# Kernel optimization log

Hardware: AMD Instinct MI355X
Metric: run time of the kernel (lower is better)

The kernel has to match this reference:

```python
import jax, jax.numpy as jnp
import numpy as np

B, C, CI, H, W = 8, 256, 64, 64, 64  # batch, in_channels, inter_channels, spatial


def conv1x1(x, w, b):
    # x: [B,C,H,W], w: [O,C] (1x1 kernel), b: [O]
    return jnp.einsum('bchw,oc->bohw', x, w) + b[None, :, None, None]


def setup_inputs() -> dict:
    key = jax.random.key(0)
    ks = jax.random.split(key, 9)
    s_in = 1.0 / np.sqrt(C)
    s_ci = 1.0 / np.sqrt(CI)
    return {
        'x': jax.random.normal(ks[0], (B, C, H, W), dtype=jnp.float32),
        'g_w': jax.random.uniform(ks[1], (CI, C), jnp.float32, -s_in, s_in),
        'g_b': jax.random.uniform(ks[2], (CI,), jnp.float32, -s_in, s_in),
        'theta_w': jax.random.uniform(ks[3], (CI, C), jnp.float32, -s_in, s_in),
        'theta_b': jax.random.uniform(ks[4], (CI,), jnp.float32, -s_in, s_in),
        'phi_w': jax.random.uniform(ks[5], (CI, C), jnp.float32, -s_in, s_in),
        'phi_b': jax.random.uniform(ks[6], (CI,), jnp.float32, -s_in, s_in),
        'w_w': jax.random.uniform(ks[7], (C, CI), jnp.float32, -s_ci, s_ci),
        'w_b': jax.random.uniform(ks[8], (C,), jnp.float32, -s_ci, s_ci),
    }


def reference(x, g_w, g_b, theta_w, theta_b, phi_w, phi_b, w_w, w_b):
    b, c, h, w = x.shape
    n = h * w
    # 1x1 conv projections, flattened over spatial positions -> [B, N, CI]
    g_x = conv1x1(x, g_w, g_b).reshape(b, CI, n).transpose(0, 2, 1)
    theta_x = conv1x1(x, theta_w, theta_b).reshape(b, CI, n).transpose(0, 2, 1)
    phi_x = conv1x1(x, phi_w, phi_b).reshape(b, CI, n)  # [B, CI, N]
    # Full non-scaled attention over spatial positions
    f = jnp.einsum('bnc,bcm->bnm', theta_x, phi_x)       # [B, N, N]
    f_div_c = jax.nn.softmax(f, axis=-1)
    y = jnp.einsum('bnm,bmc->bnc', f_div_c, g_x)         # [B, N, CI]
    y = y.transpose(0, 2, 1).reshape(b, CI, h, w)
    w_y = conv1x1(y, w_w, w_b)                            # [B, C, H, W]
    return w_y + x
```

## Files before the change

kernel.cpp:

```cpp
#include <hip/hip_runtime.h>
#include <hip/hip_bf16.h>

#define B_  8
#define C_  256
#define CI_ 64
#define N_  4096
#define KSPLIT 4
#define KTILES (N_ / 64 / KSPLIT)

typedef short short8  __attribute__((ext_vector_type(8)));
typedef short sh4     __attribute__((ext_vector_type(4)));
typedef float floatx4 __attribute__((ext_vector_type(4)));

#define LOG2E 1.4426950408889634f

__device__ __forceinline__ unsigned short f2bf(float f) {
    unsigned u = __builtin_bit_cast(unsigned, f);
    u += 0x7FFFu + ((u >> 16) & 1u);
    return (unsigned short)(u >> 16);
}
__device__ __forceinline__ float bf2f(unsigned short h) {
    unsigned u = ((unsigned)h) << 16;
    return __builtin_bit_cast(float, u);
}

__device__ __forceinline__ unsigned pk2(float a, float b) {
#if __has_builtin(__builtin_amdgcn_cvt_pk_bf16_f32)
    auto r = __builtin_amdgcn_cvt_pk_bf16_f32(a, b);
    return __builtin_bit_cast(unsigned, r);
#else
    return (unsigned)f2bf(a) | ((unsigned)f2bf(b) << 16);
#endif
}

__device__ __forceinline__ floatx4 mfma32(short8 a, short8 b, floatx4 c) {
    return __builtin_amdgcn_mfma_f32_16x16x32_bf16(a, b, c, 0, 0, 0);
}
__device__ __forceinline__ floatx4 mfma16(sh4 a, sh4 b, floatx4 c) {
#if __has_builtin(__builtin_amdgcn_mfma_f32_16x16x16bf16_1k)
    return __builtin_amdgcn_mfma_f32_16x16x16bf16_1k(a, b, c, 0, 0, 0);
#else
    floatx4 d;
    asm("v_mfma_f32_16x16x16_bf16 %0, %1, %2, %3" : "=v"(d) : "v"(a), "v"(b), "v"(c));
    return d;
#endif
}

__global__ __launch_bounds__(512, 4) void proj_kernel(
    const float* __restrict__ x,
    const float* __restrict__ wg, const float* __restrict__ bg,
    const float* __restrict__ wt, const float* __restrict__ bt,
    const float* __restrict__ wp, const float* __restrict__ bp,
    unsigned short* __restrict__ gws,
    unsigned short* __restrict__ tws,
    unsigned short* __restrict__ pws)
{
    constexpr int WS = 40;
    constexpr int GS = 72;
    __shared__ __align__(16) unsigned short wsl[2][192 * WS];
    __shared__ __align__(16) unsigned short gt[64 * GS];

    const int t    = threadIdx.x;
    const int lane = t & 63;
    const int w    = t >> 6;
    const int nf   = w >> 1;
    const int oh   = w & 1;
    const int l15  = lane & 15;
    const int quad = lane >> 4;
    const int n0   = blockIdx.x * 64;
    const int b    = blockIdx.y;

    floatx4 acc[6];
#pragma unroll
    for (int i = 0; i < 6; ++i) { floatx4 z = {0.f, 0.f, 0.f, 0.f}; acc[i] = z; }

    const int nA = n0 + nf * 16 + l15;
    const float* xbase = x + (size_t)b * C_ * N_ + nA;

    float xv[64];
#pragma unroll
    for (int kk = 0; kk < 8; ++kk)
#pragma unroll
        for (int j = 0; j < 8; ++j)
            xv[kk * 8 + j] = xbase[(size_t)(kk * 32 + quad * 8 + j) * N_];

#pragma unroll
    for (int it = 0; it < 3; ++it) {
        int u = t + it * 512;
        int row = u >> 3, c4 = u & 7;
        const float* src = (row < 64)  ? (wg + row * C_)
                         : (row < 128) ? (wt + (row - 64) * C_)
                                       : (wp + (row - 128) * C_);
        const float sc = (row >= 64 && row < 128) ? LOG2E : 1.0f;
        float4 v = *(const float4*)(src + c4 * 4);
        uint2 uu = { pk2(v.x * sc, v.y * sc), pk2(v.z * sc, v.w * sc) };
        *(uint2*)&wsl[0][row * WS + c4 * 4] = uu;
    }
    __syncthreads();

    for (int kk = 0; kk < 8; ++kk) {
        uint4 au = { pk2(xv[kk * 8 + 0], xv[kk * 8 + 1]),
                     pk2(xv[kk * 8 + 2], xv[kk * 8 + 3]),
                     pk2(xv[kk * 8 + 4], xv[kk * 8 + 5]),
                     pk2(xv[kk * 8 + 6], xv[kk * 8 + 7]) };
        short8 af = __builtin_bit_cast(short8, au);

        if (kk < 7) {
#pragma unroll
            for (int it = 0; it < 3; ++it) {
                int u = t + it * 512;
                int row = u >> 3, c4 = u & 7;
                const float* src = (row < 64)  ? (wg + row * C_)
                                 : (row < 128) ? (wt + (row - 64) * C_)
                                               : (wp + (row - 128) * C_);
                const float sc = (row >= 64 && row < 128) ? LOG2E : 1.0f;
                float4 v = *(const float4*)(src + (kk + 1) * 32 + c4 * 4);
                uint2 uu = { pk2(v.x * sc, v.y * sc), pk2(v.z * sc, v.w * sc) };
                *(uint2*)&wsl[(kk + 1) & 1][row * WS + c4 * 4] = uu;
            }
        }

#pragma unroll
        for (int oti = 0; oti < 6; ++oti) {
            const int ot = oh * 6 + oti;
            short8 bf = *(const short8*)&wsl[kk & 1][(ot * 16 + l15) * WS + quad * 8];
            acc[oti] = mfma32(af, bf, acc[oti]);
        }
        __syncthreads();
    }

#pragma unroll
    for (int oti = 0; oti < 6; ++oti) {
        const int ot = oh * 6 + oti;
        const int oc = ot * 16 + l15;
        const float bias = (ot < 4) ? bg[oc]
                         : (ot < 8) ? bt[oc - 64] * LOG2E
                                    : bp[oc - 128];
        if (ot < 4) {
#pragma unroll
            for (int r = 0; r < 4; ++r)
                gt[oc * GS + nf * 16 + quad * 4 + r] = f2bf(acc[oti][r] + bias);
        } else {
            unsigned short* dst = (ot < 8) ? tws : pws;
            const int ci = (ot < 8) ? (oc - 64) : (oc - 128);
#pragma unroll
            for (int r = 0; r < 4; ++r) {
                int n = n0 + nf * 16 + quad * 4 + r;
                dst[((size_t)b * N_ + n) * CI_ + ci] = f2bf(acc[oti][r] + bias);
            }
        }
    }
    __syncthreads();
    {
        int ci = t >> 3, n8 = t & 7;
        uint4 v = *(const uint4*)&gt[ci * GS + n8 * 8];
        *(uint4*)(gws + ((size_t)b * CI_ + ci) * N_ + n0 + n8 * 8) = v;
    }
}

__global__ __launch_bounds__(256, 4) void attn_kernel(
    const unsigned short* __restrict__ gws,
    const unsigned short* __restrict__ tws,
    const unsigned short* __restrict__ pws,
    unsigned short* __restrict__ Opart,
    float* __restrict__ lpart)
{
    constexpr int LDW = 72;
    __shared__ __align__(16) unsigned short Vs[2][64 * LDW];

    const int t    = threadIdx.x;
    const int lane = t & 63;
    const int w    = t >> 6;
    const int l15  = lane & 15;
    const int quad = lane >> 4;
    const int b    = blockIdx.x;
    const int q0   = blockIdx.y * 128;
    const int sp   = blockIdx.z;

    const int srow = t >> 3;
    const int sc8  = t & 7;

    const unsigned short* kslice = pws + ((size_t)b * N_ + sp * (N_ / KSPLIT)) * CI_;
    const unsigned short* vbase  =
        gws + ((size_t)b * CI_ + srow) * N_ + sp * (N_ / KSPLIT) + sc8 * 8;

    short8 qf[2][2];
#pragma unroll
    for (int qg = 0; qg < 2; ++qg) {
        const unsigned short* qrow =
            tws + ((size_t)b * N_ + q0 + w * 32 + qg * 16 + l15) * CI_;
        qf[qg][0] = *(const short8*)(qrow + quad * 8);
        qf[qg][1] = *(const short8*)(qrow + 32 + quad * 8);
    }

    {
        uint4 v0 = *(const uint4*)(vbase);
        uint4 v1 = *(const uint4*)(vbase + 32 * N_);
        *(uint4*)&Vs[0][srow * LDW + sc8 * 8]        = v0;
        *(uint4*)&Vs[0][(srow + 32) * LDW + sc8 * 8] = v1;
    }
    __syncthreads();

    sh4 ones4;
#pragma unroll
    for (int j = 0; j < 4; ++j) ones4[j] = (short)0x3F80;

    floatx4 Oacc[2][4], lacc[2];
    { floatx4 z = {0.f, 0.f, 0.f, 0.f};
      lacc[0] = z; lacc[1] = z;
#pragma unroll
      for (int qg = 0; qg < 2; ++qg)
#pragma unroll
          for (int f = 0; f < 4; ++f) Oacc[qg][f] = z; }

    for (int j = 0; j < KTILES; ++j) {
        const int p  = j & 1;
        const int jn = (j + 1) & (KTILES - 1);

        uint4 pv0 = *(const uint4*)(vbase + jn * 64);
        uint4 pv1 = *(const uint4*)(vbase + 32 * N_ + jn * 64);

        const unsigned short* kt = kslice + (size_t)j * 64 * CI_;
        short8 ka[4][2];
#pragma unroll
        for (int f = 0; f < 4; ++f) {
            ka[f][0] = *(const short8*)(kt + (f * 16 + l15) * CI_ + quad * 8);
            ka[f][1] = *(const short8*)(kt + (f * 16 + l15) * CI_ + 32 + quad * 8);
        }

#pragma unroll
        for (int f = 0; f < 4; ++f) {
            sh4 pfr[2];
#pragma unroll
            for (int qg = 0; qg < 2; ++qg) {
                floatx4 s = {0.f, 0.f, 0.f, 0.f};
                s = mfma32(ka[f][0], qf[qg][0], s);
                s = mfma32(ka[f][1], qf[qg][1], s);
                uint2 uu = { pk2(__builtin_amdgcn_exp2f(s[0]),
                                 __builtin_amdgcn_exp2f(s[1])),
                             pk2(__builtin_amdgcn_exp2f(s[2]),
                                 __builtin_amdgcn_exp2f(s[3])) };
                pfr[qg] = __builtin_bit_cast(sh4, uu);
                lacc[qg] = mfma16(pfr[qg], ones4, lacc[qg]);
            }
#pragma unroll
            for (int fc = 0; fc < 4; ++fc) {
                sh4 vb = *(const sh4*)&Vs[p][(fc * 16 + l15) * LDW + f * 16 + quad * 4];
#pragma unroll
                for (int qg = 0; qg < 2; ++qg)
                    Oacc[qg][fc] = mfma16(pfr[qg], vb, Oacc[qg][fc]);
            }
        }

        *(uint4*)&Vs[1 - p][srow * LDW + sc8 * 8]        = pv0;
        *(uint4*)&Vs[1 - p][(srow + 32) * LDW + sc8 * 8] = pv1;

        __syncthreads();
    }

#pragma unroll
    for (int qg = 0; qg < 2; ++qg) {
#pragma unroll
        for (int r = 0; r < 4; ++r) {
            int row = q0 + w * 32 + qg * 16 + quad * 4 + r;
            size_t obase = ((size_t)(sp * B_ + b) * N_ + row) * CI_;
#pragma unroll
            for (int fc = 0; fc < 4; ++fc)
                Opart[obase + fc * 16 + l15] = f2bf(Oacc[qg][fc][r]);
            if (l15 == 0)
                lpart[(size_t)(sp * B_ + b) * N_ + row] = lacc[qg][r];
        }
    }
}

__global__ __launch_bounds__(256, 4) void out_kernel(
    const unsigned short* __restrict__ Opart,
    const float* __restrict__ lpart,
    const float* __restrict__ ww,
    const float* __restrict__ wb,
    const float* __restrict__ x,
    float* __restrict__ out)
{
    constexpr int WS = 72;
    constexpr int TS = 66;
    __shared__ __align__(16) char smem[128 * TS * 4];
    unsigned short* wws = (unsigned short*)smem;
    float*          T   = (float*)smem;

    const int t    = threadIdx.x;
    const int lane = t & 63;
    const int w    = t >> 6;
    const int l15  = lane & 15;
    const int quad = lane >> 4;
    const int n0   = blockIdx.x * 64;
    const int b    = blockIdx.y;
    const int ch   = blockIdx.z;

#pragma unroll
    for (int it = 0; it < 8; ++it) {
        int u = t + it * 256;
        int row = u >> 4, c4 = u & 15;
        float4 v = *(const float4*)(ww + (ch * 128 + row) * CI_ + c4 * 4);
        uint2 uu = { pk2(v.x, v.y), pk2(v.z, v.w) };
        *(uint2*)&wws[row * WS + c4 * 4] = uu;
    }
    __syncthreads();

    floatx4 acc[8];
#pragma unroll
    for (int ot = 0; ot < 8; ++ot) { floatx4 z = {0.f, 0.f, 0.f, 0.f}; acc[ot] = z; }

    const int nB = n0 + w * 16 + l15;
    float lsum = 0.f;
#pragma unroll
    for (int sp = 0; sp < KSPLIT; ++sp)
        lsum += lpart[(size_t)(sp * B_ + b) * N_ + nB];
    const float inv = 1.f / lsum;

#pragma unroll
    for (int ks = 0; ks < 2; ++ks) {
        float ysum[8] = {0.f, 0.f, 0.f, 0.f, 0.f, 0.f, 0.f, 0.f};
#pragma unroll
        for (int sp = 0; sp < KSPLIT; ++sp) {
            short8 ov = *(const short8*)(Opart +
                ((size_t)(sp * B_ + b) * N_ + nB) * CI_ + ks * 32 + quad * 8);
#pragma unroll
            for (int e = 0; e < 8; ++e)
                ysum[e] += bf2f((unsigned short)ov[e]);
        }
        uint4 bu = { pk2(ysum[0] * inv, ysum[1] * inv),
                     pk2(ysum[2] * inv, ysum[3] * inv),
                     pk2(ysum[4] * inv, ysum[5] * inv),
                     pk2(ysum[6] * inv, ysum[7] * inv) };
        short8 bfrag = __builtin_bit_cast(short8, bu);
#pragma unroll
        for (int ot = 0; ot < 8; ++ot) {
            short8 afrag = *(const short8*)&wws[(ot * 16 + l15) * WS + ks * 32 + quad * 8];
            acc[ot] = mfma32(afrag, bfrag, acc[ot]);
        }
    }
    __syncthreads();

#pragma unroll
    for (int ot = 0; ot < 8; ++ot) {
#pragma unroll
        for (int r = 0; r < 4; ++r) {
            int cr = ot * 16 + quad * 4 + r;
            T[cr * TS + w * 16 + l15] = acc[ot][r] + wb[ch * 128 + cr];
        }
    }
    __syncthreads();

    const int c0 = t >> 4;
    const int nq = t & 15;
#pragma unroll
    for (int i = 0; i < 8; ++i) {
        int cr = c0 + 16 * i;
        float4 tv = *(const float4*)&T[cr * TS + nq * 4];
        size_t idx = ((size_t)b * C_ + ch * 128 + cr) * N_ + n0 + nq * 4;
        float4 xv = *(const float4*)(x + idx);
        float4 ov = { tv.x + xv.x, tv.y + xv.y, tv.z + xv.z, tv.w + xv.w };
        *(float4*)(out + idx) = ov;
    }
}

extern "C" void kernel_launch(void* const* d_in, const int* in_sizes, int n_in,
                              void* d_out, int out_size, void* d_ws, size_t ws_size,
                              hipStream_t stream) {
    const float* x  = (const float*)d_in[0];
    const float* gw = (const float*)d_in[1];
    const float* gb = (const float*)d_in[2];
    const float* tw = (const float*)d_in[3];
    const float* tb = (const float*)d_in[4];
    const float* pw = (const float*)d_in[5];
    const float* pb = (const float*)d_in[6];
    const float* ww = (const float*)d_in[7];
    const float* wb = (const float*)d_in[8];
    float* out = (float*)d_out;

    char* ws = (char*)d_ws;
    unsigned short* gws   = (unsigned short*)(ws);
    unsigned short* tws   = (unsigned short*)(ws + (4  << 20));
    unsigned short* pws   = (unsigned short*)(ws + (8  << 20));
    unsigned short* Opart = (unsigned short*)(ws + (12 << 20));
    float*          lpart = (float*)        (ws + (28 << 20));

    proj_kernel<<<dim3(64, 8), 512, 0, stream>>>(x, gw, gb, tw, tb, pw, pb, gws, tws, pws);
    attn_kernel<<<dim3(8, 32, KSPLIT), 256, 0, stream>>>(gws, tws, pws, Opart, lpart);
    out_kernel<<<dim3(64, 8, 2), 256, 0, stream>>>(Opart, lpart, ww, wb, x, out);
}
```

Baseline: 187.7 us.

## Restructure projection and output kernels to smaller tiles; prefetch K in attention

The projection kernel now works on 32-position tiles with 256 threads. It stages a transposed bf16 copy of x in shared memory and streams weight rows from global memory straight into registers, replacing the previous register-held x with shared-memory weights. The attention kernel software-pipelines the K fragment loads: the next tile's K is fetched after the current scores are exponentiated, to hide global-load latency. The output kernel also moves to 32-position tiles with a 2x2 warp split, doubling the grid for more parallelism. The cost is more blocks, reloading weights per block, and higher register pressure from the buffered fragments.

Result: slower. 209.2 us (+11.5%).

```diff
diff --git a/kernel.cpp b/kernel.cpp
--- a/kernel.cpp
+++ b/kernel.cpp
@@ -23,7 +23,6 @@
     unsigned u = ((unsigned)h) << 16;
     return __builtin_bit_cast(float, u);
 }
-
 __device__ __forceinline__ unsigned pk2(float a, float b) {
 #if __has_builtin(__builtin_amdgcn_cvt_pk_bf16_f32)
     auto r = __builtin_amdgcn_cvt_pk_bf16_f32(a, b);
@@ -32,7 +31,11 @@
     return (unsigned)f2bf(a) | ((unsigned)f2bf(b) << 16);
 #endif
 }
-
+__device__ __forceinline__ short8 pack8(float4 a, float4 b, float sc) {
+    uint4 u = { pk2(a.x * sc, a.y * sc), pk2(a.z * sc, a.w * sc),
+                pk2(b.x * sc, b.y * sc), pk2(b.z * sc, b.w * sc) };
+    return __builtin_bit_cast(short8, u);
+}
 __device__ __forceinline__ floatx4 mfma32(short8 a, short8 b, floatx4 c) {
     return __builtin_amdgcn_mfma_f32_16x16x32_bf16(a, b, c, 0, 0, 0);
 }
@@ -46,7 +49,7 @@
 #endif
 }
 
-__global__ __launch_bounds__(512, 4) void proj_kernel(
+__global__ __launch_bounds__(256, 4) void proj_kernel(
     const float* __restrict__ x,
     const float* __restrict__ wg, const float* __restrict__ bg,
     const float* __restrict__ wt, const float* __restrict__ bt,
@@ -55,106 +58,119 @@
     unsigned short* __restrict__ tws,
     unsigned short* __restrict__ pws)
 {
-    constexpr int WS = 40;
-    constexpr int GS = 72;
-    __shared__ __align__(16) unsigned short wsl[2][192 * WS];
+    constexpr int XK = 40;
+    constexpr int GS = 40;
+    __shared__ __align__(16) unsigned short xt[2][32 * XK];
     __shared__ __align__(16) unsigned short gt[64 * GS];
 
     const int t    = threadIdx.x;
     const int lane = t & 63;
     const int w    = t >> 6;
-    const int nf   = w >> 1;
-    const int oh   = w & 1;
     const int l15  = lane & 15;
     const int quad = lane >> 4;
-    const int n0   = blockIdx.x * 64;
+    const int n0   = blockIdx.x * 32;
     const int b    = blockIdx.y;
 
-    floatx4 acc[6];
-#pragma unroll
-    for (int i = 0; i < 6; ++i) { floatx4 z = {0.f, 0.f, 0.f, 0.f}; acc[i] = z; }
-
-    const int nA = n0 + nf * 16 + l15;
-    const float* xbase = x + (size_t)b * C_ * N_ + nA;
-
-    float xv[64];
-#pragma unroll
-    for (int kk = 0; kk < 8; ++kk)
-#pragma unroll
-        for (int j = 0; j < 8; ++j)
-            xv[kk * 8 + j] = xbase[(size_t)(kk * 32 + quad * 8 + j) * N_];
-
-#pragma unroll
-    for (int it = 0; it < 3; ++it) {
-        int u = t + it * 512;
-        int row = u >> 3, c4 = u & 7;
-        const float* src = (row < 64)  ? (wg + row * C_)
-                         : (row < 128) ? (wt + (row - 64) * C_)
-                                       : (wp + (row - 128) * C_);
-        const float sc = (row >= 64 && row < 128) ? LOG2E : 1.0f;
-        float4 v = *(const float4*)(src + c4 * 4);
-        uint2 uu = { pk2(v.x * sc, v.y * sc), pk2(v.z * sc, v.w * sc) };
-        *(uint2*)&wsl[0][row * WS + c4 * 4] = uu;
-    }
+    const float* wrow[3];
+    float wsc[3];
+    int   frag[3];
+#pragma unroll
+    for (int of = 0; of < 3; ++of) {
+        int fr = w * 3 + of;
+        frag[of] = fr;
+        if (fr < 4)      { wrow[of] = wg + (fr * 16 + l15) * C_;          wsc[of] = 1.0f; }
+        else if (fr < 8) { wrow[of] = wt + ((fr - 4) * 16 + l15) * C_;    wsc[of] = LOG2E; }
+        else             { wrow[of] = wp + ((fr - 8) * 16 + l15) * C_;    wsc[of] = 1.0f; }
+    }
+
+    floatx4 acc[3][2];
+#pragma unroll
+    for (int of = 0; of < 3; ++of)
+#pragma unroll
+        for (int nf = 0; nf < 2; ++nf) { floatx4 z = {0.f,0.f,0.f,0.f}; acc[of][nf] = z; }
+
+    const int xr = t >> 3;
+    const int xc = t & 7;
+    const float* xsrc = x + ((size_t)b * C_ + xr) * N_ + n0 + xc * 4;
+
+    float4 xv = *(const float4*)(xsrc);
+    float4 wcur[3][2];
+#pragma unroll
+    for (int of = 0; of < 3; ++of) {
+        wcur[of][0] = *(const float4*)(wrow[of] + quad * 8);
+        wcur[of][1] = *(const float4*)(wrow[of] + quad * 8 + 4);
+    }
+    xt[0][(xc * 4 + 0) * XK + xr] = f2bf(xv.x);
+    xt[0][(xc * 4 + 1) * XK + xr] = f2bf(xv.y);
+    xt[0][(xc * 4 + 2) * XK + xr] = f2bf(xv.z);
+    xt[0][(xc * 4 + 3) * XK + xr] = f2bf(xv.w);
     __syncthreads();
 
     for (int kk = 0; kk < 8; ++kk) {
-        uint4 au = { pk2(xv[kk * 8 + 0], xv[kk * 8 + 1]),
-                     pk2(xv[kk * 8 + 2], xv[kk * 8 + 3]),
-                     pk2(xv[kk * 8 + 4], xv[kk * 8 + 5]),
-                     pk2(xv[kk * 8 + 6], xv[kk * 8 + 7]) };
-        short8 af = __builtin_bit_cast(short8, au);
-
+        float4 xn;
+        float4 wn[3][2];
         if (kk < 7) {
-#pragma unroll
-            for (int it = 0; it < 3; ++it) {
-                int u = t + it * 512;
-                int row = u >> 3, c4 = u & 7;
-                const float* src = (row < 64)  ? (wg + row * C_)
-                                 : (row < 128) ? (wt + (row - 64) * C_)
-                                               : (wp + (row - 128) * C_);
-                const float sc = (row >= 64 && row < 128) ? LOG2E : 1.0f;
-                float4 v = *(const float4*)(src + (kk + 1) * 32 + c4 * 4);
-                uint2 uu = { pk2(v.x * sc, v.y * sc), pk2(v.z * sc, v.w * sc) };
-                *(uint2*)&wsl[(kk + 1) & 1][row * WS + c4 * 4] = uu;
+            xn = *(const float4*)(xsrc + (size_t)(kk + 1) * 32 * N_);
+#pragma unroll
+            for (int of = 0; of < 3; ++of) {
+                wn[of][0] = *(const float4*)(wrow[of] + (kk + 1) * 32 + quad * 8);
+                wn[of][1] = *(const float4*)(wrow[of] + (kk + 1) * 32 + quad * 8 + 4);
             }
         }
 
-#pragma unroll
-        for (int oti = 0; oti < 6; ++oti) {
-            const int ot = oh * 6 + oti;
-            short8 bf = *(const short8*)&wsl[kk & 1][(ot * 16 + l15) * WS + quad * 8];
-            acc[oti] = mfma32(af, bf, acc[oti]);
+        short8 bf[3];
+#pragma unroll
+        for (int of = 0; of < 3; ++of)
+            bf[of] = pack8(wcur[of][0], wcur[of][1], wsc[of]);
+
+#pragma unroll
+        for (int nf = 0; nf < 2; ++nf) {
+            short8 af = *(const short8*)&xt[kk & 1][(nf * 16 + l15) * XK + quad * 8];
+#pragma unroll
+            for (int of = 0; of < 3; ++of)
+                acc[of][nf] = mfma32(af, bf[of], acc[of][nf]);
+        }
+
+        if (kk < 7) {
+            xt[(kk + 1) & 1][(xc * 4 + 0) * XK + xr] = f2bf(xn.x);
+            xt[(kk + 1) & 1][(xc * 4 + 1) * XK + xr] = f2bf(xn.y);
+            xt[(kk + 1) & 1][(xc * 4 + 2) * XK + xr] = f2bf(xn.z);
+            xt[(kk + 1) & 1][(xc * 4 + 3) * XK + xr] = f2bf(xn.w);
         }
         __syncthreads();
-    }
-
-#pragma unroll
-    for (int oti = 0; oti < 6; ++oti) {
-        const int ot = oh * 6 + oti;
-        const int oc = ot * 16 + l15;
-        const float bias = (ot < 4) ? bg[oc]
-                         : (ot < 8) ? bt[oc - 64] * LOG2E
-                                    : bp[oc - 128];
-        if (ot < 4) {
-#pragma unroll
-            for (int r = 0; r < 4; ++r)
-                gt[oc * GS + nf * 16 + quad * 4 + r] = f2bf(acc[oti][r] + bias);
+#pragma unroll
+        for (int of = 0; of < 3; ++of) { wcur[of][0] = wn[of][0]; wcur[of][1] = wn[of][1]; }
+    }
+
+#pragma unroll
+    for (int of = 0; of < 3; ++of) {
+        const int fr = frag[of];
+        if (fr < 4) {
+            const int oc = fr * 16 + l15;
+            const float bias = bg[oc];
+#pragma unroll
+            for (int nf = 0; nf < 2; ++nf)
+#pragma unroll
+                for (int r = 0; r < 4; ++r)
+                    gt[oc * GS + nf * 16 + quad * 4 + r] = f2bf(acc[of][nf][r] + bias);
         } else {
-            unsigned short* dst = (ot < 8) ? tws : pws;
-            const int ci = (ot < 8) ? (oc - 64) : (oc - 128);
-#pragma unroll
-            for (int r = 0; r < 4; ++r) {
-                int n = n0 + nf * 16 + quad * 4 + r;
-                dst[((size_t)b * N_ + n) * CI_ + ci] = f2bf(acc[oti][r] + bias);
-            }
+            const int ci = (fr < 8) ? ((fr - 4) * 16 + l15) : ((fr - 8) * 16 + l15);
+            const float bias = (fr < 8) ? bt[ci] * LOG2E : bp[ci];
+            unsigned short* dst = (fr < 8) ? tws : pws;
+#pragma unroll
+            for (int nf = 0; nf < 2; ++nf)
+#pragma unroll
+                for (int r = 0; r < 4; ++r) {
+                    int n = n0 + nf * 16 + quad * 4 + r;
+                    dst[((size_t)b * N_ + n) * CI_ + ci] = f2bf(acc[of][nf][r] + bias);
+                }
         }
     }
     __syncthreads();
     {
-        int ci = t >> 3, n8 = t & 7;
-        uint4 v = *(const uint4*)&gt[ci * GS + n8 * 8];
-        *(uint4*)(gws + ((size_t)b * CI_ + ci) * N_ + n0 + n8 * 8) = v;
+        int ci = t >> 2, cq = t & 3;
+        uint4 v = *(const uint4*)&gt[ci * GS + cq * 8];
+        *(uint4*)(gws + ((size_t)b * CI_ + ci) * N_ + n0 + cq * 8) = v;
     }
 }
 
@@ -193,9 +209,15 @@
         qf[qg][1] = *(const short8*)(qrow + 32 + quad * 8);
     }
 
+    short8 ka[4][2];
     {
         uint4 v0 = *(const uint4*)(vbase);
         uint4 v1 = *(const uint4*)(vbase + 32 * N_);
+#pragma unroll
+        for (int f = 0; f < 4; ++f) {
+            ka[f][0] = *(const short8*)(kslice + (f * 16 + l15) * CI_ + quad * 8);
+            ka[f][1] = *(const short8*)(kslice + (f * 16 + l15) * CI_ + 32 + quad * 8);
+        }
         *(uint4*)&Vs[0][srow * LDW + sc8 * 8]        = v0;
         *(uint4*)&Vs[0][(srow + 32) * LDW + sc8 * 8] = v1;
     }
@@ -203,7 +225,7 @@
 
     sh4 ones4;
 #pragma unroll
-    for (int j = 0; j < 4; ++j) ones4[j] = (short)0x3F80;
+    for (int j4 = 0; j4 < 4; ++j4) ones4[j4] = (short)0x3F80;
 
     floatx4 Oacc[2][4], lacc[2];
     { floatx4 z = {0.f, 0.f, 0.f, 0.f};
@@ -220,17 +242,9 @@
         uint4 pv0 = *(const uint4*)(vbase + jn * 64);
         uint4 pv1 = *(const uint4*)(vbase + 32 * N_ + jn * 64);
 
-        const unsigned short* kt = kslice + (size_t)j * 64 * CI_;
-        short8 ka[4][2];
+        sh4 pfr[4][2];
 #pragma unroll
         for (int f = 0; f < 4; ++f) {
-            ka[f][0] = *(const short8*)(kt + (f * 16 + l15) * CI_ + quad * 8);
-            ka[f][1] = *(const short8*)(kt + (f * 16 + l15) * CI_ + 32 + quad * 8);
-        }
-
-#pragma unroll
-        for (int f = 0; f < 4; ++f) {
-            sh4 pfr[2];
 #pragma unroll
             for (int qg = 0; qg < 2; ++qg) {
                 floatx4 s = {0.f, 0.f, 0.f, 0.f};
@@ -240,15 +254,30 @@
                                  __builtin_amdgcn_exp2f(s[1])),
                              pk2(__builtin_amdgcn_exp2f(s[2]),
                                  __builtin_amdgcn_exp2f(s[3])) };
-                pfr[qg] = __builtin_bit_cast(sh4, uu);
-                lacc[qg] = mfma16(pfr[qg], ones4, lacc[qg]);
+                pfr[f][qg] = __builtin_bit_cast(sh4, uu);
             }
+        }
+
+        {
+            const unsigned short* kt = kslice + (size_t)jn * 64 * CI_;
+#pragma unroll
+            for (int f = 0; f < 4; ++f) {
+                ka[f][0] = *(const short8*)(kt + (f * 16 + l15) * CI_ + quad * 8);
+                ka[f][1] = *(const short8*)(kt + (f * 16 + l15) * CI_ + 32 + quad * 8);
+            }
+        }
+
+#pragma unroll
+        for (int f = 0; f < 4; ++f) {
+#pragma unroll
+            for (int qg = 0; qg < 2; ++qg)
+                lacc[qg] = mfma16(pfr[f][qg], ones4, lacc[qg]);
 #pragma unroll
             for (int fc = 0; fc < 4; ++fc) {
                 sh4 vb = *(const sh4*)&Vs[p][(fc * 16 + l15) * LDW + f * 16 + quad * 4];
 #pragma unroll
                 for (int qg = 0; qg < 2; ++qg)
-                    Oacc[qg][fc] = mfma16(pfr[qg], vb, Oacc[qg][fc]);
+                    Oacc[qg][fc] = mfma16(pfr[f][qg], vb, Oacc[qg][fc]);
             }
         }
 
@@ -282,8 +311,8 @@
     float* __restrict__ out)
 {
     constexpr int WS = 72;
-    constexpr int TS = 66;
-    __shared__ __align__(16) char smem[128 * TS * 4];
+    constexpr int TS = 36;
+    __shared__ __align__(16) char smem[128 * WS * 2];
     unsigned short* wws = (unsigned short*)smem;
     float*          T   = (float*)smem;
 
@@ -292,9 +321,11 @@
     const int w    = t >> 6;
     const int l15  = lane & 15;
     const int quad = lane >> 4;
-    const int n0   = blockIdx.x * 64;
+    const int n0   = blockIdx.x * 32;
     const int b    = blockIdx.y;
     const int ch   = blockIdx.z;
+    const int nf   = w & 1;
+    const int oh   = w >> 1;
 
 #pragma unroll
     for (int it = 0; it < 8; ++it) {
@@ -306,11 +337,11 @@
     }
     __syncthreads();
 
-    floatx4 acc[8];
-#pragma unroll
-    for (int ot = 0; ot < 8; ++ot) { floatx4 z = {0.f, 0.f, 0.f, 0.f}; acc[ot] = z; }
-
-    const int nB = n0 + w * 16 + l15;
+    floatx4 acc[4];
+#pragma unroll
+    for (int ot = 0; ot < 4; ++ot) { floatx4 z = {0.f, 0.f, 0.f, 0.f}; acc[ot] = z; }
+
+    const int nB = n0 + nf * 16 + l15;
     float lsum = 0.f;
 #pragma unroll
     for (int sp = 0; sp < KSPLIT; ++sp)
@@ -334,30 +365,29 @@
                      pk2(ysum[6] * inv, ysum[7] * inv) };
         short8 bfrag = __builtin_bit_cast(short8, bu);
 #pragma unroll
-        for (int ot = 0; ot < 8; ++ot) {
-            short8 afrag = *(const short8*)&wws[(ot * 16 + l15) * WS + ks * 32 + quad * 8];
+        for (int ot = 0; ot < 4; ++ot) {
+            short8 afrag = *(const short8*)&wws[(oh * 64 + ot * 16 + l15) * WS + ks * 32 + quad * 8];
             acc[ot] = mfma32(afrag, bfrag, acc[ot]);
         }
     }
     __syncthreads();
 
 #pragma unroll
-    for (int ot = 0; ot < 8; ++ot) {
+    for (int ot = 0; ot < 4; ++ot) {
 #pragma unroll
         for (int r = 0; r < 4; ++r) {
-            int cr = ot * 16 + quad * 4 + r;
-            T[cr * TS + w * 16 + l15] = acc[ot][r] + wb[ch * 128 + cr];
-        }
-    }
-    __syncthreads();
-
-    const int c0 = t >> 4;
-    const int nq = t & 15;
-#pragma unroll
-    for (int i = 0; i < 8; ++i) {
-        int cr = c0 + 16 * i;
-        float4 tv = *(const float4*)&T[cr * TS + nq * 4];
-        size_t idx = ((size_t)b * C_ + ch * 128 + cr) * N_ + n0 + nq * 4;
+            int cr = oh * 64 + ot * 16 + quad * 4 + r;
+            T[cr * TS + nf * 16 + l15] = acc[ot][r] + wb[ch * 128 + cr];
+        }
+    }
+    __syncthreads();
+
+#pragma unroll
+    for (int it = 0; it < 4; ++it) {
+        int u = t + it * 256;
+        int row = u >> 3, col = u & 7;
+        float4 tv = *(const float4*)&T[row * TS + col * 4];
+        size_t idx = ((size_t)b * C_ + ch * 128 + row) * N_ + n0 + col * 4;
         float4 xv = *(const float4*)(x + idx);
         float4 ov = { tv.x + xv.x, tv.y + xv.y, tv.z + xv.z, tv.w + xv.w };
         *(float4*)(out + idx) = ov;
@@ -385,7 +415,7 @@
     unsigned short* Opart = (unsigned short*)(ws + (12 << 20));
     float*          lpart = (float*)        (ws + (28 << 20));
 
-    proj_kernel<<<dim3(64, 8), 512, 0, stream>>>(x, gw, gb, tw, tb, pw, pb, gws, tws, pws);
+    proj_kernel<<<dim3(128, 8), 256, 0, stream>>>(x, gw, gb, tw, tb, pw, pb, gws, tws, pws);
     attn_kernel<<<dim3(8, 32, KSPLIT), 256, 0, stream>>>(gws, tws, pws, Opart, lpart);
-    out_kernel<<<dim3(64, 8, 2), 256, 0, stream>>>(Opart, lpart, ww, wb, x, out);
-}
+    out_kernel<<<dim3(128, 8, 2), 256, 0, stream>>>(Opart, lpart, ww, wb, x, out);
+}
```
